# Kernel tuning notes

Measured on AMD Instinct MI355X. Metric: run time of the kernel, lower is better.

The kernel has to match this reference:

```python
import jax, jax.numpy as jnp
import numpy as np

N_NODES = 50000
N_EDGES = 800000
D_IN = 128
D_HID = 128
D_OUT = 40
NUM_LAYERS = 2


def _sage_conv(x, src, dst, W_l, b_l, W_r, num_nodes):
    # PyG SAGEConv (aggr='mean'): out = lin_l(mean_{j in N(i)} x_j) + lin_r(x_i)
    msg = x[src]                                              # [E, d] gather
    agg = jax.ops.segment_sum(msg, dst, num_segments=num_nodes)  # [N, d] scatter-add
    deg = jax.ops.segment_sum(jnp.ones_like(dst, dtype=x.dtype), dst,
                              num_segments=num_nodes)
    agg = agg / jnp.clip(deg, 1.0)[:, None]                   # mean (deg>=1 clamp)
    return agg @ W_l.T + b_l + x @ W_r.T


def setup_inputs() -> dict:
    key = jax.random.key(0)
    ks = jax.random.split(key, 10)
    x = jax.random.normal(ks[0], (N_NODES, D_IN), dtype=jnp.float32)
    edge_index = jax.random.randint(ks[1], (2, N_EDGES), 0, N_NODES, dtype=jnp.int64)
    s = 1.0 / np.sqrt(D_IN)
    W1_l = jax.random.uniform(ks[2], (D_HID, D_IN), jnp.float32, -s, s)
    b1_l = jax.random.uniform(ks[3], (D_HID,), jnp.float32, -s, s)
    W1_r = jax.random.uniform(ks[4], (D_HID, D_IN), jnp.float32, -s, s)
    sh = 1.0 / np.sqrt(D_HID)
    W2_l = jax.random.uniform(ks[5], (D_HID, D_HID), jnp.float32, -sh, sh)
    b2_l = jax.random.uniform(ks[6], (D_HID,), jnp.float32, -sh, sh)
    W2_r = jax.random.uniform(ks[7], (D_HID, D_HID), jnp.float32, -sh, sh)
    sc = 1.0 / np.sqrt(D_HID * NUM_LAYERS)
    W_lin = jax.random.uniform(ks[8], (D_OUT, D_HID * NUM_LAYERS), jnp.float32, -sc, sc)
    b_lin = jax.random.uniform(ks[9], (D_OUT,), jnp.float32, -sc, sc)
    return {"x": x, "edge_index": edge_index,
            "W1_l": W1_l, "b1_l": b1_l, "W1_r": W1_r,
            "W2_l": W2_l, "b2_l": b2_l, "W2_r": W2_r,
            "W_lin": W_lin, "b_lin": b_lin}


def reference(x, edge_index, W1_l, b1_l, W1_r, W2_l, b2_l, W2_r, W_lin, b_lin):
    src, dst = edge_index[0], edge_index[1]
    n = x.shape[0]
    h1 = jax.nn.relu(_sage_conv(x, src, dst, W1_l, b1_l, W1_r, n))   # dropout: eval mode -> identity
    h2 = jax.nn.relu(_sage_conv(h1, src, dst, W2_l, b2_l, W2_r, n))
    h_cat = jnp.concatenate([h1, h2], axis=1)                        # [N, 2*hid]
    logits = h_cat @ W_lin.T + b_lin                                 # [N, out]
    return jax.nn.log_softmax(logits, axis=1)
```

## Files before the change

kernel.cpp:

```cpp
#include <hip/hip_runtime.h>
#include <math.h>

#define N_NODES 50000
#define N_EDGES 800000
#define D 128
#define NBLK 196

typedef __attribute__((ext_vector_type(8))) short bf16x8;
typedef __attribute__((ext_vector_type(4))) float f32x4;

static __device__ __forceinline__ unsigned short f2bf(float f) {
    unsigned int u = __float_as_uint(f);
    u = (u + 0x7fffu + ((u >> 16) & 1u)) >> 16;
    return (unsigned short)u;
}
static __device__ __forceinline__ float bf2f(unsigned short h) {
    return __uint_as_float(((unsigned int)h) << 16);
}

__global__ void prep_deg_kernel(const int* __restrict__ dst, int* __restrict__ deg,
                                int* __restrict__ rank,
                                const float* __restrict__ x,
                                const float* __restrict__ W1l, const float* __restrict__ W1r,
                                const float* __restrict__ W2l, const float* __restrict__ W2r,
                                const float* __restrict__ Wlin,
                                unsigned short* __restrict__ xhi, unsigned short* __restrict__ xlo,
                                unsigned short* __restrict__ W1hi, unsigned short* __restrict__ W1lo,
                                unsigned short* __restrict__ W2hi, unsigned short* __restrict__ W2lo,
                                unsigned short* __restrict__ WLhi, unsigned short* __restrict__ WLlo) {
    int b = blockIdx.x, tid = threadIdx.x;
    if (b < 3125) {
        int e = b * 256 + tid;
        rank[e] = atomicAdd(&deg[dst[e]], 1);
    } else if (b < 9375) {
        int i = ((b - 3125) * 256 + tid) * 4;
        float4 v = *(const float4*)(x + i);
        ushort4 h, l;
        h.x = f2bf(v.x); l.x = f2bf(v.x - bf2f(h.x));
        h.y = f2bf(v.y); l.y = f2bf(v.y - bf2f(h.y));
        h.z = f2bf(v.z); l.z = f2bf(v.z - bf2f(h.z));
        h.w = f2bf(v.w); l.w = f2bf(v.w - bf2f(h.w));
        *(ushort4*)(xhi + i) = h;
        *(ushort4*)(xlo + i) = l;
    } else if (b < 9503) {
        int isW2 = (b >= 9439);
        const float* A = isW2 ? W2l : W1l;
        const float* B = isW2 ? W2r : W1r;
        unsigned short* hi = isW2 ? W2hi : W1hi;
        unsigned short* lo = isW2 ? W2lo : W1lo;
        int f = (b - (isW2 ? 9439 : 9375)) * 2 + (tid >> 7);
        int t = tid & 127;
        float va = A[f * 128 + t], vb = B[f * 128 + t];
        unsigned short ha = f2bf(va), hb = f2bf(vb);
        hi[f * 256 + t]       = ha;
        hi[f * 256 + 128 + t] = hb;
        lo[f * 256 + t]       = f2bf(va - bf2f(ha));
        lo[f * 256 + 128 + t] = f2bf(vb - bf2f(hb));
    } else {
        int f = b - 9503;
        float v = (f < 40) ? Wlin[f * 256 + tid] : 0.f;
        unsigned short h = f2bf(v);
        WLhi[f * 256 + tid] = h;
        WLlo[f * 256 + tid] = f2bf(v - bf2f(h));
    }
}

__global__ void scan_partial(const int* __restrict__ deg, int* __restrict__ bsum) {
    __shared__ int wt[4];
    int tid = threadIdx.x, lane = tid & 63, wv = tid >> 6;
    int idx = blockIdx.x * 256 + tid;
    int v = (idx < N_NODES) ? deg[idx] : 0;
    int s = v;
    #pragma unroll
    for (int o = 1; o < 64; o <<= 1) s += __shfl_xor(s, o, 64);
    if (lane == 0) wt[wv] = s;
    __syncthreads();
    if (tid == 0) bsum[blockIdx.x] = wt[0] + wt[1] + wt[2] + wt[3];
}

__global__ void scan_write(const int* __restrict__ deg, const int* __restrict__ bsum,
                           int* __restrict__ rowptr) {
    __shared__ int wt[4], wt2[4];
    int tid = threadIdx.x, lane = tid & 63, wv = tid >> 6;
    int v0 = (tid < blockIdx.x) ? bsum[tid] : 0;
    int s0 = v0;
    #pragma unroll
    for (int o = 1; o < 64; o <<= 1) s0 += __shfl_xor(s0, o, 64);
    if (lane == 0) wt2[wv] = s0;
    int idx = blockIdx.x * 256 + tid;
    int v = (idx < N_NODES) ? deg[idx] : 0;
    int s = v;
    #pragma unroll
    for (int o = 1; o < 64; o <<= 1) { int t = __shfl_up(s, o, 64); if (lane >= o) s += t; }
    if (lane == 63) wt[wv] = s;
    __syncthreads();
    int boff = wt2[0] + wt2[1] + wt2[2] + wt2[3];
    #pragma unroll
    for (int w = 0; w < 4; w++) boff += (w < wv) ? wt[w] : 0;
    int excl = boff + s - v;
    if (idx < N_NODES) rowptr[idx] = excl;
    if (idx == 0) rowptr[N_NODES] = N_EDGES;
}

__global__ void bucket_kernel(const int* __restrict__ src, const int* __restrict__ dst,
                              const int* __restrict__ rowptr, const int* __restrict__ rank,
                              int* __restrict__ srcs_sorted) {
    int e = blockIdx.x * blockDim.x + threadIdx.x;
    if (e < N_EDGES) {
        srcs_sorted[rowptr[dst[e]] + rank[e]] = src[e];
    }
}

template<bool FINAL>
__global__ __launch_bounds__(512, 4) void fused_layer(
    const int* __restrict__ srcs, const int* __restrict__ rowptr,
    const unsigned short* __restrict__ Shi,
    const unsigned short* __restrict__ A2hi, const unsigned short* __restrict__ A2lo,
    const unsigned short* __restrict__ Whi, const unsigned short* __restrict__ Wlo,
    const float* __restrict__ bias,
    unsigned short* __restrict__ Ohi, unsigned short* __restrict__ Olo,
    const unsigned short* __restrict__ WLhi, const unsigned short* __restrict__ WLlo,
    const float* __restrict__ blin, float* __restrict__ out)
{
    __shared__ unsigned int Ah[64 * 68];
    __shared__ unsigned int Al[64 * 68];
    __shared__ unsigned short Wl[8192];
    __shared__ float stats[256];

    const int tid = threadIdx.x;
    const int wv = tid >> 6, lane = tid & 63;
    const int nb0 = blockIdx.x * 64;

    const unsigned int* xp = (const unsigned int*)Shi;
    #pragma unroll 1
    for (int it = 0; it < 4; it++) {
        int nlA = it * 16 + wv, nlB = nlA + 8;
        int nodeA = min(nb0 + nlA, N_NODES - 1);
        int nodeB = min(nb0 + nlB, N_NODES - 1);
        int begA = rowptr[nodeA], endA = rowptr[nodeA + 1];
        int begB = rowptr[nodeB], endB = rowptr[nodeB + 1];
        int nA = (endA - begA + 15) >> 4;
        int nB = (endB - begB + 15) >> 4;
        int nmax = max(nA, nB);
        float axA[4] = {0,0,0,0}, ayA[4] = {0,0,0,0};
        float axB[4] = {0,0,0,0}, ayB[4] = {0,0,0,0};
        #pragma unroll 1
        for (int b = 0; b < nmax; b++) {
            unsigned int uA[16], uB[16];
            int baseA = begA + b * 16, baseB = begB + b * 16;
            if (b < nA) {
                #pragma unroll
                for (int j = 0; j < 16; j++) {
                    int ee = min(baseA + j, endA - 1);
                    uA[j] = xp[(size_t)srcs[ee] * 64 + lane];
                }
            }
            if (b < nB) {
                #pragma unroll
                for (int j = 0; j < 16; j++) {
                    int ee = min(baseB + j, endB - 1);
                    uB[j] = xp[(size_t)srcs[ee] * 64 + lane];
                }
            }
            if (b < nA) {
                int cA = min(16, endA - baseA);
                #pragma unroll
                for (int j = 0; j < 16; j++) {
                    if (j < cA) {
                        axA[j & 3] += __uint_as_float(uA[j] << 16);
                        ayA[j & 3] += __uint_as_float(uA[j] & 0xffff0000u);
                    }
                }
            }
            if (b < nB) {
                int cB = min(16, endB - baseB);
                #pragma unroll
                for (int j = 0; j < 16; j++) {
                    if (j < cB) {
                        axB[j & 3] += __uint_as_float(uB[j] << 16);
                        ayB[j & 3] += __uint_as_float(uB[j] & 0xffff0000u);
                    }
                }
            }
        }
        {
            float sx = (axA[0] + axA[1]) + (axA[2] + axA[3]);
            float sy = (ayA[0] + ayA[1]) + (ayA[2] + ayA[3]);
            float inv = 1.0f / fmaxf((float)(endA - begA), 1.0f);
            sx *= inv; sy *= inv;
            unsigned short h0 = f2bf(sx), h1 = f2bf(sy);
            unsigned short l0 = f2bf(sx - bf2f(h0)), l1 = f2bf(sy - bf2f(h1));
            Ah[nlA * 68 + lane] = (unsigned int)h0 | ((unsigned int)h1 << 16);
            Al[nlA * 68 + lane] = (unsigned int)l0 | ((unsigned int)l1 << 16);
        }
        {
            float sx = (axB[0] + axB[1]) + (axB[2] + axB[3]);
            float sy = (ayB[0] + ayB[1]) + (ayB[2] + ayB[3]);
            float inv = 1.0f / fmaxf((float)(endB - begB), 1.0f);
            sx *= inv; sy *= inv;
            unsigned short h0 = f2bf(sx), h1 = f2bf(sy);
            unsigned short l0 = f2bf(sx - bf2f(h0)), l1 = f2bf(sy - bf2f(h1));
            Ah[nlB * 68 + lane] = (unsigned int)h0 | ((unsigned int)h1 << 16);
            Al[nlB * 68 + lane] = (unsigned int)l0 | ((unsigned int)l1 << 16);
        }
    }
    __syncthreads();

    const int m = lane & 15, quad = lane >> 4;
    const int g = wv & 3, tp = wv >> 2;
    const int node_base = nb0 + g * 16;
    const int nodec = min(node_base + m, N_NODES - 1);

    bf16x8 a1h[4], a1l[4], a2h[4], a2l[4];
    {
        const unsigned short* r2h = A2hi + (size_t)nodec * D + quad * 8;
        const unsigned short* r2l = A2lo + (size_t)nodec * D + quad * 8;
        #pragma unroll
        for (int ks = 0; ks < 4; ks++) {
            a2h[ks] = *(const bf16x8*)(r2h + ks * 32);
            a2l[ks] = *(const bf16x8*)(r2l + ks * 32);
        }
        #pragma unroll
        for (int ks = 0; ks < 4; ks++) {
            int ad = ((g * 16 + m) * 68 + quad * 4 + ks * 16) * 2;
            a1h[ks] = *(const bf16x8*)((const unsigned short*)Ah + ad);
            a1l[ks] = *(const bf16x8*)((const unsigned short*)Al + ad);
        }
    }

    #pragma unroll 1
    for (int fq = 0; fq < 4; fq++) {
        const int f0 = fq * 32;
        if (fq) __syncthreads();
        #pragma unroll
        for (int itS = 0; itS < 2; itS++) {
            int c = tid + itS * 512;
            int nt = c >> 9, w2 = c & 511;
            int ks = w2 >> 6, lidx = w2 & 63;
            int mm = lidx >> 2, qq = lidx & 3;
            const unsigned short* gp = Whi + (size_t)(f0 + nt * 16 + mm) * 256 + ks * 32 + qq * 8;
            *(bf16x8*)&Wl[(size_t)c * 8] = *(const bf16x8*)gp;
        }
        __syncthreads();

        int f = f0 + tp * 16 + m;
        const unsigned short* wlorow = Wlo + (size_t)f * 256 + quad * 8;
        f32x4 acc0 = {0.f, 0.f, 0.f, 0.f};
        f32x4 acc1 = {0.f, 0.f, 0.f, 0.f};
        f32x4 acc2 = {0.f, 0.f, 0.f, 0.f};
        #pragma unroll
        for (int ks = 0; ks < 8; ks++) {
            bf16x8 bh = *(const bf16x8*)&Wl[(size_t)(((tp * 8 + ks) << 6) + (m * 4 + quad)) * 8];
            bf16x8 bl = *(const bf16x8*)(wlorow + ks * 32);
            bf16x8 ah = (ks < 4) ? a1h[ks] : a2h[ks - 4];
            bf16x8 al = (ks < 4) ? a1l[ks] : a2l[ks - 4];
            acc0 = __builtin_amdgcn_mfma_f32_16x16x32_bf16(ah, bh, acc0, 0, 0, 0);
            acc1 = __builtin_amdgcn_mfma_f32_16x16x32_bf16(ah, bl, acc1, 0, 0, 0);
            acc2 = __builtin_amdgcn_mfma_f32_16x16x32_bf16(al, bh, acc2, 0, 0, 0);
        }
        float bv = bias[f];
        #pragma unroll
        for (int r = 0; r < 4; r++) {
            int lrow = g * 16 + quad * 4 + r;
            int nrow = nb0 + lrow;
            float v = fmaxf((acc0[r] + (acc1[r] + acc2[r])) + bv, 0.f);
            unsigned short h = f2bf(v);
            unsigned short l = f2bf(v - bf2f(h));
            if (FINAL) {
                ((unsigned short*)Ah)[lrow * 136 + f] = h;
                ((unsigned short*)Al)[lrow * 136 + f] = l;
            } else if (nrow < N_NODES) {
                Ohi[(size_t)nrow * D + f] = h;
                Olo[(size_t)nrow * D + f] = l;
            }
        }
    }

    if (!FINAL) return;

    __syncthreads();
    bf16x8 a3h[4], a3l[4];
    #pragma unroll
    for (int ks = 0; ks < 4; ks++) {
        int ad = (g * 16 + m) * 136 + ks * 32 + quad * 8;
        a3h[ks] = *(const bf16x8*)((const unsigned short*)Ah + ad);
        a3l[ks] = *(const bf16x8*)((const unsigned short*)Al + ad);
    }
    const int ntiles = (tp == 0) ? 2 : 1;
    float res[2][4];
    #pragma unroll
    for (int t = 0; t < 2; t++) {
        if (t >= ntiles) break;
        int nt = (tp == 0) ? t : 2;
        int f = nt * 16 + m;
        const unsigned short* whirow = WLhi + (size_t)f * 256 + quad * 8;
        const unsigned short* wlorow = WLlo + (size_t)f * 256 + quad * 8;
        f32x4 acc0 = {0.f, 0.f, 0.f, 0.f};
        f32x4 acc1 = {0.f, 0.f, 0.f, 0.f};
        f32x4 acc2 = {0.f, 0.f, 0.f, 0.f};
        #pragma unroll
        for (int ks = 0; ks < 8; ks++) {
            bf16x8 bh = *(const bf16x8*)(whirow + ks * 32);
            bf16x8 bl = *(const bf16x8*)(wlorow + ks * 32);
            bf16x8 ah = (ks < 4) ? a2h[ks] : a3h[ks - 4];
            bf16x8 al = (ks < 4) ? a2l[ks] : a3l[ks - 4];
            acc0 = __builtin_amdgcn_mfma_f32_16x16x32_bf16(ah, bh, acc0, 0, 0, 0);
            acc1 = __builtin_amdgcn_mfma_f32_16x16x32_bf16(ah, bl, acc1, 0, 0, 0);
            acc2 = __builtin_amdgcn_mfma_f32_16x16x32_bf16(al, bh, acc2, 0, 0, 0);
        }
        float bv = (f < 40) ? blin[f] : 0.f;
        #pragma unroll
        for (int r = 0; r < 4; r++) res[t][r] = (acc0[r] + (acc1[r] + acc2[r])) + bv;
    }
    #pragma unroll
    for (int r = 0; r < 4; r++) {
        float pm = -INFINITY;
        #pragma unroll
        for (int t = 0; t < 2; t++) {
            if (t >= ntiles) break;
            int f = ((tp == 0) ? t : 2) * 16 + m;
            if (f < 40) pm = fmaxf(pm, res[t][r]);
        }
        #pragma unroll
        for (int o = 8; o > 0; o >>= 1) pm = fmaxf(pm, __shfl_xor(pm, o, 64));
        if (m == 0) stats[tp * 64 + g * 16 + quad * 4 + r] = pm;
    }
    __syncthreads();
    float gm[4];
    #pragma unroll
    for (int r = 0; r < 4; r++) {
        int row = g * 16 + quad * 4 + r;
        gm[r] = fmaxf(stats[row], stats[64 + row]);
        float ps = 0.f;
        #pragma unroll
        for (int t = 0; t < 2; t++) {
            if (t >= ntiles) break;
            int f = ((tp == 0) ? t : 2) * 16 + m;
            if (f < 40) ps += expf(res[t][r] - gm[r]);
        }
        #pragma unroll
        for (int o = 8; o > 0; o >>= 1) ps += __shfl_xor(ps, o, 64);
        if (m == 0) stats[128 + tp * 64 + row] = ps;
    }
    __syncthreads();
    #pragma unroll
    for (int r = 0; r < 4; r++) {
        int row = g * 16 + quad * 4 + r;
        int nrow = nb0 + row;
        if (nrow >= N_NODES) continue;
        float lse = gm[r] + logf(stats[128 + row] + stats[192 + row]);
        #pragma unroll
        for (int t = 0; t < 2; t++) {
            if (t >= ntiles) break;
            int f = ((tp == 0) ? t : 2) * 16 + m;
            if (f < 40) out[(size_t)nrow * 40 + f] = res[t][r] - lse;
        }
    }
}

extern "C" void kernel_launch(void* const* d_in, const int* in_sizes, int n_in,
                              void* d_out, int out_size, void* d_ws, size_t ws_size,
                              hipStream_t stream) {
    const float* x     = (const float*)d_in[0];
    const int*   ei    = (const int*)d_in[1];
    const int*   src   = ei;
    const int*   dst   = ei + N_EDGES;
    const float* W1_l  = (const float*)d_in[2];
    const float* b1_l  = (const float*)d_in[3];
    const float* W1_r  = (const float*)d_in[4];
    const float* W2_l  = (const float*)d_in[5];
    const float* b2_l  = (const float*)d_in[6];
    const float* W2_r  = (const float*)d_in[7];
    const float* W_lin = (const float*)d_in[8];
    const float* b_lin = (const float*)d_in[9];
    float* out = (float*)d_out;

    const size_t nd = (size_t)N_NODES * D;
    unsigned short* xhi  = (unsigned short*)d_ws;
    unsigned short* xlo  = xhi + nd;
    unsigned short* h1hi = xlo + nd;
    unsigned short* h1lo = h1hi + nd;
    unsigned short* W1hi = h1lo + nd;
    unsigned short* W1lo = W1hi + 128 * 256;
    unsigned short* W2hi = W1lo + 128 * 256;
    unsigned short* W2lo = W2hi + 128 * 256;
    unsigned short* WLhi = W2lo + 128 * 256;
    unsigned short* WLlo = WLhi + 48 * 256;
    int* deg    = (int*)(WLlo + 48 * 256);
    int* rowptr = deg + N_NODES;
    int* rank   = rowptr + N_NODES + 1;
    int* srcs_sorted = rank + N_EDGES;
    int* bsum   = srcs_sorted + N_EDGES;

    hipMemsetAsync(deg, 0, N_NODES * sizeof(int), stream);
    prep_deg_kernel<<<9551, 256, 0, stream>>>(dst, deg, rank, x, W1_l, W1_r, W2_l, W2_r, W_lin,
                                              xhi, xlo, W1hi, W1lo, W2hi, W2lo, WLhi, WLlo);

    scan_partial<<<NBLK, 256, 0, stream>>>(deg, bsum);
    scan_write<<<NBLK, 256, 0, stream>>>(deg, bsum, rowptr);
    bucket_kernel<<<(N_EDGES + 255) / 256, 256, 0, stream>>>(src, dst, rowptr, rank, srcs_sorted);

    const int lblk = (N_NODES + 63) / 64;

    fused_layer<false><<<lblk, 512, 0, stream>>>(srcs_sorted, rowptr, xhi, xhi, xlo,
                                                 W1hi, W1lo, b1_l, h1hi, h1lo,
                                                 nullptr, nullptr, nullptr, nullptr);
    fused_layer<true><<<lblk, 512, 0, stream>>>(srcs_sorted, rowptr, h1hi, h1hi, h1lo,
                                                W2hi, W2lo, b2_l, nullptr, nullptr,
                                                WLhi, WLlo, b_lin, out);
}
```

Measured before the change: 332.5 us.

## Drop LDS weight staging, load W directly from global; raise occupancy bound

Removes the shared-memory staging of the high-part weight tile and the per-quarter barriers, reading Whi rows straight from global memory (L2-cached) like Wlo. The launch bound's min-blocks hint rises from 4 to 8, limiting registers per thread to allow more resident waves. Each wave's rowptr loads are replaced by one coalesced per-lane load plus wave shuffles, and gather address math uses 32-bit byte offsets. The trade-off is more global and L2 traffic for weights, and possible register spills under the tighter occupancy bound.

```diff
diff --git a/kernel.cpp b/kernel.cpp
--- a/kernel.cpp
+++ b/kernel.cpp
@@ -112,7 +112,7 @@
 }
 
 template<bool FINAL>
-__global__ __launch_bounds__(512, 4) void fused_layer(
+__global__ __launch_bounds__(512, 8) void fused_layer(
     const int* __restrict__ srcs, const int* __restrict__ rowptr,
     const unsigned short* __restrict__ Shi,
     const unsigned short* __restrict__ A2hi, const unsigned short* __restrict__ A2lo,
@@ -124,21 +124,23 @@
 {
     __shared__ unsigned int Ah[64 * 68];
     __shared__ unsigned int Al[64 * 68];
-    __shared__ unsigned short Wl[8192];
     __shared__ float stats[256];
 
     const int tid = threadIdx.x;
     const int wv = tid >> 6, lane = tid & 63;
     const int nb0 = blockIdx.x * 64;
 
-    const unsigned int* xp = (const unsigned int*)Shi;
+    const int nclamp = min(nb0 + lane, N_NODES - 1);
+    const int rp0 = rowptr[nclamp];
+    const int rp1 = rowptr[nclamp + 1];
+
+    const char* xb = (const char*)Shi;
+    const int lb = lane << 2;
     #pragma unroll 1
     for (int it = 0; it < 4; it++) {
         int nlA = it * 16 + wv, nlB = nlA + 8;
-        int nodeA = min(nb0 + nlA, N_NODES - 1);
-        int nodeB = min(nb0 + nlB, N_NODES - 1);
-        int begA = rowptr[nodeA], endA = rowptr[nodeA + 1];
-        int begB = rowptr[nodeB], endB = rowptr[nodeB + 1];
+        int begA = __shfl(rp0, nlA, 64), endA = __shfl(rp1, nlA, 64);
+        int begB = __shfl(rp0, nlB, 64), endB = __shfl(rp1, nlB, 64);
         int nA = (endA - begA + 15) >> 4;
         int nB = (endB - begB + 15) >> 4;
         int nmax = max(nA, nB);
@@ -152,14 +154,14 @@
                 #pragma unroll
                 for (int j = 0; j < 16; j++) {
                     int ee = min(baseA + j, endA - 1);
-                    uA[j] = xp[(size_t)srcs[ee] * 64 + lane];
+                    uA[j] = *(const unsigned int*)(xb + (((unsigned)srcs[ee] << 8) + lb));
                 }
             }
             if (b < nB) {
                 #pragma unroll
                 for (int j = 0; j < 16; j++) {
                     int ee = min(baseB + j, endB - 1);
-                    uB[j] = xp[(size_t)srcs[ee] * 64 + lane];
+                    uB[j] = *(const unsigned int*)(xb + (((unsigned)srcs[ee] << 8) + lb));
                 }
             }
             if (b < nA) {
@@ -227,30 +229,19 @@
             a1l[ks] = *(const bf16x8*)((const unsigned short*)Al + ad);
         }
     }
+    if (FINAL) __syncthreads();
 
     #pragma unroll 1
     for (int fq = 0; fq < 4; fq++) {
-        const int f0 = fq * 32;
-        if (fq) __syncthreads();
-        #pragma unroll
-        for (int itS = 0; itS < 2; itS++) {
-            int c = tid + itS * 512;
-            int nt = c >> 9, w2 = c & 511;
-            int ks = w2 >> 6, lidx = w2 & 63;
-            int mm = lidx >> 2, qq = lidx & 3;
-            const unsigned short* gp = Whi + (size_t)(f0 + nt * 16 + mm) * 256 + ks * 32 + qq * 8;
-            *(bf16x8*)&Wl[(size_t)c * 8] = *(const bf16x8*)gp;
-        }
-        __syncthreads();
-
-        int f = f0 + tp * 16 + m;
+        const int f = fq * 32 + tp * 16 + m;
+        const unsigned short* whirow = Whi + (size_t)f * 256 + quad * 8;
         const unsigned short* wlorow = Wlo + (size_t)f * 256 + quad * 8;
         f32x4 acc0 = {0.f, 0.f, 0.f, 0.f};
         f32x4 acc1 = {0.f, 0.f, 0.f, 0.f};
         f32x4 acc2 = {0.f, 0.f, 0.f, 0.f};
         #pragma unroll
         for (int ks = 0; ks < 8; ks++) {
-            bf16x8 bh = *(const bf16x8*)&Wl[(size_t)(((tp * 8 + ks) << 6) + (m * 4 + quad)) * 8];
+            bf16x8 bh = *(const bf16x8*)(whirow + ks * 32);
             bf16x8 bl = *(const bf16x8*)(wlorow + ks * 32);
             bf16x8 ah = (ks < 4) ? a1h[ks] : a2h[ks - 4];
             bf16x8 al = (ks < 4) ? a1l[ks] : a2l[ks - 4];
```

After: 545.1 us. 63.9% more time.

## Gather neighbor rows with 16-byte loads, 4 edges per wave, shuffled src indices

Applied to the files above, without the earlier changes.

Restructures the mean-aggregation gather. Each wave now loads 64 source indices cooperatively and broadcasts them with shuffles. Each 16-lane group fetches a full 256-byte bf16 row with 16-byte vector loads, so four edges are processed per iteration, and partial sums are reduced across groups with xor shuffles. Rowptr values are also loaded once per block and shuffled instead of being reloaded per node. The aim is fewer, wider memory transactions and less serial index loading, at the cost of extra shuffle reductions and masked tail lanes.

```diff
diff --git a/kernel.cpp b/kernel.cpp
--- a/kernel.cpp
+++ b/kernel.cpp
@@ -8,6 +8,7 @@
 
 typedef __attribute__((ext_vector_type(8))) short bf16x8;
 typedef __attribute__((ext_vector_type(4))) float f32x4;
+typedef __attribute__((ext_vector_type(4))) unsigned int u32x4;
 
 static __device__ __forceinline__ unsigned short f2bf(float f) {
     unsigned int u = __float_as_uint(f);
@@ -131,84 +132,104 @@
     const int wv = tid >> 6, lane = tid & 63;
     const int nb0 = blockIdx.x * 64;
 
-    const unsigned int* xp = (const unsigned int*)Shi;
+    const int nclamp = min(nb0 + lane, N_NODES - 1);
+    const int rp0 = rowptr[nclamp];
+    const int rp1 = rowptr[nclamp + 1];
+
+    const char* xb = (const char*)Shi;
+    const int g = lane >> 4;
+    const int q = lane & 15;
+    const int qb = q << 4;
     #pragma unroll 1
     for (int it = 0; it < 4; it++) {
         int nlA = it * 16 + wv, nlB = nlA + 8;
-        int nodeA = min(nb0 + nlA, N_NODES - 1);
-        int nodeB = min(nb0 + nlB, N_NODES - 1);
-        int begA = rowptr[nodeA], endA = rowptr[nodeA + 1];
-        int begB = rowptr[nodeB], endB = rowptr[nodeB + 1];
-        int nA = (endA - begA + 15) >> 4;
-        int nB = (endB - begB + 15) >> 4;
-        int nmax = max(nA, nB);
-        float axA[4] = {0,0,0,0}, ayA[4] = {0,0,0,0};
-        float axB[4] = {0,0,0,0}, ayB[4] = {0,0,0,0};
+        int begA = __shfl(rp0, nlA, 64), endA = __shfl(rp1, nlA, 64);
+        int begB = __shfl(rp0, nlB, 64), endB = __shfl(rp1, nlB, 64);
+        int degA = endA - begA, degB = endB - begB;
+        float ax[4] = {0,0,0,0}, ay[4] = {0,0,0,0};
+        float bx[4] = {0,0,0,0}, by[4] = {0,0,0,0};
+        int nsA = (degA + 63) >> 6, nsB = (degB + 63) >> 6;
+        int nsmax = max(nsA, nsB);
         #pragma unroll 1
-        for (int b = 0; b < nmax; b++) {
-            unsigned int uA[16], uB[16];
-            int baseA = begA + b * 16, baseB = begB + b * 16;
-            if (b < nA) {
-                #pragma unroll
-                for (int j = 0; j < 16; j++) {
-                    int ee = min(baseA + j, endA - 1);
-                    uA[j] = xp[(size_t)srcs[ee] * 64 + lane];
+        for (int st = 0; st < nsmax; st++) {
+            int svA = 0, svB = 0;
+            int nbA = 0, nbB = 0;
+            if (st < nsA) {
+                int sb = begA + (st << 6);
+                nbA = min(64, endA - sb);
+                svA = srcs[min(sb + lane, endA - 1)];
+            }
+            if (st < nsB) {
+                int sb = begB + (st << 6);
+                nbB = min(64, endB - sb);
+                svB = srcs[min(sb + lane, endB - 1)];
+            }
+            int itA = (nbA + 3) >> 2, itB = (nbB + 3) >> 2;
+            int itmax = max(itA, itB);
+            #pragma unroll 4
+            for (int b = 0; b < itmax; b++) {
+                int ei = (b << 2) + g;
+                if (b < itA) {
+                    unsigned srcv = (unsigned)__shfl(svA, ei, 64);
+                    u32x4 v = *(const u32x4*)(xb + ((srcv << 8) + qb));
+                    v.x = (ei < nbA) ? v.x : 0u;
+                    v.y = (ei < nbA) ? v.y : 0u;
+                    v.z = (ei < nbA) ? v.z : 0u;
+                    v.w = (ei < nbA) ? v.w : 0u;
+                    ax[0] += __uint_as_float(v.x << 16); ay[0] += __uint_as_float(v.x & 0xffff0000u);
+                    ax[1] += __uint_as_float(v.y << 16); ay[1] += __uint_as_float(v.y & 0xffff0000u);
+                    ax[2] += __uint_as_float(v.z << 16); ay[2] += __uint_as_float(v.z & 0xffff0000u);
+                    ax[3] += __uint_as_float(v.w << 16); ay[3] += __uint_as_float(v.w & 0xffff0000u);
+                }
+                if (b < itB) {
+                    unsigned srcv = (unsigned)__shfl(svB, ei, 64);
+                    u32x4 v = *(const u32x4*)(xb + ((srcv << 8) + qb));
+                    v.x = (ei < nbB) ? v.x : 0u;
+                    v.y = (ei < nbB) ? v.y : 0u;
+                    v.z = (ei < nbB) ? v.z : 0u;
+                    v.w = (ei < nbB) ? v.w : 0u;
+                    bx[0] += __uint_as_float(v.x << 16); by[0] += __uint_as_float(v.x & 0xffff0000u);
+                    bx[1] += __uint_as_float(v.y << 16); by[1] += __uint_as_float(v.y & 0xffff0000u);
+                    bx[2] += __uint_as_float(v.z << 16); by[2] += __uint_as_float(v.z & 0xffff0000u);
+                    bx[3] += __uint_as_float(v.w << 16); by[3] += __uint_as_float(v.w & 0xffff0000u);
                 }
             }
-            if (b < nB) {
-                #pragma unroll
-                for (int j = 0; j < 16; j++) {
-                    int ee = min(baseB + j, endB - 1);
-                    uB[j] = xp[(size_t)srcs[ee] * 64 + lane];
-                }
+        }
+        #pragma unroll
+        for (int d = 0; d < 4; d++) {
+            ax[d] += __shfl_xor(ax[d], 16, 64); ax[d] += __shfl_xor(ax[d], 32, 64);
+            ay[d] += __shfl_xor(ay[d], 16, 64); ay[d] += __shfl_xor(ay[d], 32, 64);
+            bx[d] += __shfl_xor(bx[d], 16, 64); bx[d] += __shfl_xor(bx[d], 32, 64);
+            by[d] += __shfl_xor(by[d], 16, 64); by[d] += __shfl_xor(by[d], 32, 64);
+        }
+        if (g == 0) {
+            float invA = 1.0f / fmaxf((float)degA, 1.0f);
+            float invB = 1.0f / fmaxf((float)degB, 1.0f);
+            u32x4 ha, la, hb, lb;
+            #pragma unroll
+            for (int d = 0; d < 4; d++) {
+                float sx = ax[d] * invA, sy = ay[d] * invA;
+                unsigned short h0 = f2bf(sx), h1 = f2bf(sy);
+                unsigned short l0 = f2bf(sx - bf2f(h0)), l1 = f2bf(sy - bf2f(h1));
+                ha[d] = (unsigned)h0 | ((unsigned)h1 << 16);
+                la[d] = (unsigned)l0 | ((unsigned)l1 << 16);
+                float tx = bx[d] * invB, ty = by[d] * invB;
+                unsigned short h2 = f2bf(tx), h3 = f2bf(ty);
+                unsigned short l2 = f2bf(tx - bf2f(h2)), l3 = f2bf(ty - bf2f(h3));
+                hb[d] = (unsigned)h2 | ((unsigned)h3 << 16);
+                lb[d] = (unsigned)l2 | ((unsigned)l3 << 16);
             }
-            if (b < nA) {
-                int cA = min(16, endA - baseA);
-                #pragma unroll
-                for (int j = 0; j < 16; j++) {
-                    if (j < cA) {
-                        axA[j & 3] += __uint_as_float(uA[j] << 16);
-                        ayA[j & 3] += __uint_as_float(uA[j] & 0xffff0000u);
-                    }
-                }
-            }
-            if (b < nB) {
-                int cB = min(16, endB - baseB);
-                #pragma unroll
-                for (int j = 0; j < 16; j++) {
-                    if (j < cB) {
-                        axB[j & 3] += __uint_as_float(uB[j] << 16);
-                        ayB[j & 3] += __uint_as_float(uB[j] & 0xffff0000u);
-                    }
-                }
-            }
-        }
-        {
-            float sx = (axA[0] + axA[1]) + (axA[2] + axA[3]);
-            float sy = (ayA[0] + ayA[1]) + (ayA[2] + ayA[3]);
-            float inv = 1.0f / fmaxf((float)(endA - begA), 1.0f);
-            sx *= inv; sy *= inv;
-            unsigned short h0 = f2bf(sx), h1 = f2bf(sy);
-            unsigned short l0 = f2bf(sx - bf2f(h0)), l1 = f2bf(sy - bf2f(h1));
-            Ah[nlA * 68 + lane] = (unsigned int)h0 | ((unsigned int)h1 << 16);
-            Al[nlA * 68 + lane] = (unsigned int)l0 | ((unsigned int)l1 << 16);
-        }
-        {
-            float sx = (axB[0] + axB[1]) + (axB[2] + axB[3]);
-            float sy = (ayB[0] + ayB[1]) + (ayB[2] + ayB[3]);
-            float inv = 1.0f / fmaxf((float)(endB - begB), 1.0f);
-            sx *= inv; sy *= inv;
-            unsigned short h0 = f2bf(sx), h1 = f2bf(sy);
-            unsigned short l0 = f2bf(sx - bf2f(h0)), l1 = f2bf(sy - bf2f(h1));
-            Ah[nlB * 68 + lane] = (unsigned int)h0 | ((unsigned int)h1 << 16);
-            Al[nlB * 68 + lane] = (unsigned int)l0 | ((unsigned int)l1 << 16);
+            *(u32x4*)&Ah[nlA * 68 + q * 4] = ha;
+            *(u32x4*)&Al[nlA * 68 + q * 4] = la;
+            *(u32x4*)&Ah[nlB * 68 + q * 4] = hb;
+            *(u32x4*)&Al[nlB * 68 + q * 4] = lb;
         }
     }
     __syncthreads();
 
     const int m = lane & 15, quad = lane >> 4;
-    const int g = wv & 3, tp = wv >> 2;
-    const int node_base = nb0 + g * 16;
+    const int gg = wv & 3, tp = wv >> 2;
+    const int node_base = nb0 + gg * 16;
     const int nodec = min(node_base + m, N_NODES - 1);
 
     bf16x8 a1h[4], a1l[4], a2h[4], a2l[4];
@@ -222,7 +243,7 @@
         }
         #pragma unroll
         for (int ks = 0; ks < 4; ks++) {
-            int ad = ((g * 16 + m) * 68 + quad * 4 + ks * 16) * 2;
+            int ad = ((gg * 16 + m) * 68 + quad * 4 + ks * 16) * 2;
             a1h[ks] = *(const bf16x8*)((const unsigned short*)Ah + ad);
             a1l[ks] = *(const bf16x8*)((const unsigned short*)Al + ad);
         }
@@ -261,7 +282,7 @@
         float bv = bias[f];
         #pragma unroll
         for (int r = 0; r < 4; r++) {
-            int lrow = g * 16 + quad * 4 + r;
+            int lrow = gg * 16 + quad * 4 + r;
             int nrow = nb0 + lrow;
             float v = fmaxf((acc0[r] + (acc1[r] + acc2[r])) + bv, 0.f);
             unsigned short h = f2bf(v);
@@ -282,7 +303,7 @@
     bf16x8 a3h[4], a3l[4];
     #pragma unroll
     for (int ks = 0; ks < 4; ks++) {
-        int ad = (g * 16 + m) * 136 + ks * 32 + quad * 8;
+        int ad = (gg * 16 + m) * 136 + ks * 32 + quad * 8;
         a3h[ks] = *(const bf16x8*)((const unsigned short*)Ah + ad);
         a3l[ks] = *(const bf16x8*)((const unsigned short*)Al + ad);
     }
@@ -323,13 +344,13 @@
         }
         #pragma unroll
         for (int o = 8; o > 0; o >>= 1) pm = fmaxf(pm, __shfl_xor(pm, o, 64));
-        if (m == 0) stats[tp * 64 + g * 16 + quad * 4 + r] = pm;
+        if (m == 0) stats[tp * 64 + gg * 16 + quad * 4 + r] = pm;
     }
     __syncthreads();
     float gm[4];
     #pragma unroll
     for (int r = 0; r < 4; r++) {
-        int row = g * 16 + quad * 4 + r;
+        int row = gg * 16 + quad * 4 + r;
         gm[r] = fmaxf(stats[row], stats[64 + row]);
         float ps = 0.f;
         #pragma unroll
@@ -345,7 +366,7 @@
     __syncthreads();
     #pragma unroll
     for (int r = 0; r < 4; r++) {
-        int row = g * 16 + quad * 4 + r;
+        int row = gg * 16 + quad * 4 + r;
         int nrow = nb0 + row;
         if (nrow >= N_NODES) continue;
         float lse = gm[r] + logf(stats[128 + row] + stats[192 + row]);
```

Result: slower. 339.7 us (+2.2%).
